# Kernel tuning notes

Hardware: AMD Instinct MI355X
Metric: run time of the kernel (lower is better)

The kernel has to match this reference:

```python
import jax, jax.numpy as jnp
import numpy as np

D_MODEL = 128
N_HEADS = 4
HEAD_DIM = D_MODEL // N_HEADS
N_LAYERS = 6
N_CELLS = 121
LN_EPS = 1e-5


def _build_hex_edges():
    # 11x11 axial hex grid -> 121 cells with 6-neighbor connectivity (640 directed edges)
    dirs = [(1, 0), (-1, 0), (0, 1), (0, -1), (1, -1), (-1, 1)]
    qr_to_idx = {(q, r): q * 11 + r for q in range(11) for r in range(11)}
    src, dst = [], []
    for (q, r), i in qr_to_idx.items():
        for dq, dr in dirs:
            j = qr_to_idx.get((q + dq, r + dr))
            if j is not None:
                src.append(i)
                dst.append(j)
    return jnp.array([src, dst], dtype=jnp.int32)


def layer_norm(x, g, b):
    m = jnp.mean(x, axis=-1, keepdims=True)
    v = jnp.mean(jnp.square(x - m), axis=-1, keepdims=True)
    return (x - m) * jax.lax.rsqrt(v + LN_EPS) * g + b


def gat_layer(h_in, edge_index, W, a_src, a_dst):
    # h_in: (B,N,d); W: (d, H*Dh); a_src/a_dst: (H,Dh)
    B, N, _ = h_in.shape
    h = (h_in @ W).reshape(B, N, N_HEADS, HEAD_DIM)
    src, dst = edge_index[0], edge_index[1]
    h_src = h[:, src]                                   # (B,E,H,Dh)
    e_src = jnp.einsum('behd,hd->beh', h_src, a_src)
    e_dst = jnp.einsum('behd,hd->beh', h[:, dst], a_dst)
    e = jax.nn.leaky_relu(e_src + e_dst, 0.2)           # (B,E,H)
    # edge softmax grouped by destination node (segment ops reduce leading axis)
    e_t = jnp.moveaxis(e, 1, 0)                         # (E,B,H)
    m = jax.ops.segment_max(e_t, dst, num_segments=N)   # (N,B,H)
    exp_e = jnp.exp(e_t - m[dst])                       # (E,B,H)
    s = jax.ops.segment_sum(exp_e, dst, num_segments=N) # (N,B,H)
    alpha = exp_e / (s[dst] + 1e-10)                    # (E,B,H)
    msgs = alpha[..., None] * jnp.moveaxis(h_src, 1, 0) # (E,B,H,Dh)
    out = jax.ops.segment_sum(msgs, dst, num_segments=N)  # (N,B,H,Dh)
    return jnp.moveaxis(out, 0, 1).reshape(B, N, N_HEADS * HEAD_DIM)


def _forward(x, enc_W, enc_b, enc_ln_g, enc_ln_b, ln1_g, ln1_b, gat_W, a_src, a_dst,
             ln2_g, ln2_b, ff_W1, ff_b1, ff_W2, ff_b2, fn_g, fn_b, edge_index):
    h = jax.nn.gelu(layer_norm(x @ enc_W + enc_b, enc_ln_g, enc_ln_b), approximate=False)
    for i in range(N_LAYERS):
        h = h + gat_layer(layer_norm(h, ln1_g[i], ln1_b[i]), edge_index,
                          gat_W[i], a_src[i], a_dst[i])
        hn = layer_norm(h, ln2_g[i], ln2_b[i])
        h = h + (jax.nn.gelu(hn @ ff_W1[i] + ff_b1[i], approximate=False) @ ff_W2[i] + ff_b2[i])
    return layer_norm(h, fn_g, fn_b)


def setup_inputs() -> dict:
    key = jax.random.key(0)
    ks = jax.random.split(key, 12)
    B, d, L, H, Dh = 256, D_MODEL, N_LAYERS, N_HEADS, HEAD_DIM
    inp = {
        'x': jax.random.uniform(ks[0], (B, N_CELLS, 6), dtype=jnp.float32),
        'enc_W': jax.random.normal(ks[1], (6, d), dtype=jnp.float32) * 0.3,
        'enc_b': jnp.zeros((d,), jnp.float32),
        'enc_ln_g': jnp.ones((d,), jnp.float32),
        'enc_ln_b': jnp.zeros((d,), jnp.float32),
        'ln1_g': jnp.ones((L, d), jnp.float32),
        'ln1_b': jnp.zeros((L, d), jnp.float32),
        'gat_W': jax.random.normal(ks[2], (L, d, H * Dh), dtype=jnp.float32) * (1.0 / np.sqrt(d)),
        'a_src': jax.random.normal(ks[3], (L, H, Dh), dtype=jnp.float32) * 0.1,
        'a_dst': jax.random.normal(ks[4], (L, H, Dh), dtype=jnp.float32) * 0.1,
        'ln2_g': jnp.ones((L, d), jnp.float32),
        'ln2_b': jnp.zeros((L, d), jnp.float32),
        'ff_W1': jax.random.normal(ks[5], (L, d, 4 * d), dtype=jnp.float32) * (1.0 / np.sqrt(d)),
        'ff_b1': jnp.zeros((L, 4 * d), jnp.float32),
        'ff_W2': jax.random.normal(ks[6], (L, 4 * d, d), dtype=jnp.float32) * (1.0 / np.sqrt(4 * d)),
        'ff_b2': jnp.zeros((L, d), jnp.float32),
        'fn_g': jnp.ones((d,), jnp.float32),
        'fn_b': jnp.zeros((d,), jnp.float32),
        'edge_index': _build_hex_edges(),
    }
    return inp


def reference(x, enc_W, enc_b, enc_ln_g, enc_ln_b, ln1_g, ln1_b, gat_W, a_src, a_dst,
              ln2_g, ln2_b, ff_W1, ff_b1, ff_W2, ff_b2, fn_g, fn_b, edge_index):
    return _forward(x, enc_W, enc_b, enc_ln_g, enc_ln_b, ln1_g, ln1_b, gat_W, a_src,
                    a_dst, ln2_g, ln2_b, ff_W1, ff_b1, ff_W2, ff_b2, fn_g, fn_b, edge_index)
```

## Files before the change

### kernel.cpp

```cpp
#include <hip/hip_runtime.h>
#include <math.h>

#define NCELL 121
#define NB 256
#define DMODEL 128
#define DFF 512
#define LNEPS 1e-5f
#define MAXDEG 8
#define ROWS (NB * NCELL)

typedef __attribute__((ext_vector_type(8))) short short8;
typedef __attribute__((ext_vector_type(4))) float f32x4;

#define MFMA(a, b, c) __builtin_amdgcn_mfma_f32_16x16x32_bf16(a, b, c, 0, 0, 0)

__device__ __forceinline__ float warp_sum64(float x) {
#pragma unroll
  for (int m = 32; m >= 1; m >>= 1) x += __shfl_xor(x, m, 64);
  return x;
}
__device__ __forceinline__ unsigned short f2bf(float f) {
  union { float f; unsigned u; } v; v.f = f;
  unsigned r = v.u + 0x7fffu + ((v.u >> 16) & 1u);
  return (unsigned short)(r >> 16);
}
__device__ __forceinline__ unsigned pack2(float a, float b) {
  return (unsigned)f2bf(a) | ((unsigned)f2bf(b) << 16);
}
__device__ __forceinline__ float bf2f(short s) {
  union { unsigned u; float f; } v;
  v.u = ((unsigned)(unsigned short)s) << 16;
  return v.f;
}
__device__ __forceinline__ float erf_fast(float x) {
  const float ax = fabsf(x);
  const float t = 1.0f / (1.0f + 0.3275911f * ax);
  const float p = t * (0.254829592f +
                  t * (-0.284496736f +
                  t * (1.421413741f +
                  t * (-1.453152027f +
                  t * 1.061405429f))));
  const float r = 1.0f - p * __expf(-ax * ax);
  return copysignf(r, x);
}
__device__ __forceinline__ float gelu_fast(float x) {
  return 0.5f * x * (1.0f + erf_fast(x * 0.70710678118654752f));
}
__device__ __forceinline__ float lrelu(float x) { return x > 0.0f ? x : 0.2f * x; }

__global__ void k_cvt(const float* __restrict__ src, short* __restrict__ dst,
                      int K, int N, int total) {
  const int i = blockIdx.x * 256 + threadIdx.x;
  if (i >= total) return;
  const int KN = K * N;
  const int layer = i / KN, rem = i % KN;
  const int n = rem / K, kk = rem % K;
  dst[i] = (short)f2bf(src[(size_t)layer * KN + (size_t)kk * N + n]);
}

__global__ void k_adj(const int* __restrict__ ei, int E,
                      int* __restrict__ deg, int* __restrict__ nbr) {
  const int node = blockIdx.x * 4 + (threadIdx.x >> 6);
  const int l = threadIdx.x & 63;
  if (node >= NCELL) return;
  const int* srcp = ei;
  const int* dstp = ei + E;
  int d = 0;
  for (int e0 = 0; e0 < E; e0 += 64) {
    const int e = e0 + l;
    const bool hit = (e < E) && (dstp[e] == node);
    const unsigned long long mb = __ballot(hit);
    if (hit) {
      const int pos = d + __popcll(mb & ((1ULL << l) - 1ULL));
      if (pos < MAXDEG) nbr[node * MAXDEG + pos] = srcp[e];
    }
    d += __popcll(mb);
  }
  if (l == 0) deg[node] = (d < MAXDEG ? d : MAXDEG);
}

__global__ __launch_bounds__(256) void k_enc(
    const float* __restrict__ x, const float* __restrict__ W,
    const float* __restrict__ bias, const float* __restrict__ g,
    const float* __restrict__ be, float* __restrict__ h) {
  const int tid = threadIdx.x, w = tid >> 6, l = tid & 63;
  const int r0 = blockIdx.x * 64;
  for (int k = 0; k < 16; k++) {
    const int gr = r0 + w * 16 + k;
    const float* xr = x + (size_t)gr * 6;
    const float x0 = xr[0], x1 = xr[1], x2 = xr[2];
    const float x3 = xr[3], x4 = xr[4], x5 = xr[5];
    const int d1 = l + 64;
    float v0 = bias[l] + x0 * W[l] + x1 * W[DMODEL + l] + x2 * W[2 * DMODEL + l]
             + x3 * W[3 * DMODEL + l] + x4 * W[4 * DMODEL + l] + x5 * W[5 * DMODEL + l];
    float v1 = bias[d1] + x0 * W[d1] + x1 * W[DMODEL + d1] + x2 * W[2 * DMODEL + d1]
             + x3 * W[3 * DMODEL + d1] + x4 * W[4 * DMODEL + d1] + x5 * W[5 * DMODEL + d1];
    const float mean = warp_sum64(v0 + v1) * (1.0f / 128.0f);
    const float e0 = v0 - mean, e1 = v1 - mean;
    const float var = warp_sum64(e0 * e0 + e1 * e1) * (1.0f / 128.0f);
    const float rs = rsqrtf(var + LNEPS);
    float* hp = h + (size_t)gr * DMODEL;
    hp[l] = gelu_fast(e0 * rs * g[l] + be[l]);
    hp[d1] = gelu_fast(e1 * rs * g[d1] + be[d1]);
  }
}

__global__ __launch_bounds__(256, 2) void k_gat_a(
    const float* __restrict__ g1, const float* __restrict__ b1,
    const short* __restrict__ Wgt, const float* __restrict__ asrc,
    const float* __restrict__ adst, const float* __restrict__ h,
    short* __restrict__ hh, float* __restrict__ es, float* __restrict__ ed) {
  __shared__ short sHn[64 * DMODEL];
  const int tid = threadIdx.x, w = tid >> 6, l = tid & 63;
  const int lane16 = l & 15, q = l >> 4;
  const int r0 = blockIdx.x * 64;

  {
    const int row = tid >> 2, sub = tid & 3;
    const float* hr = h + (size_t)(r0 + row) * DMODEL + sub * 32;
    float4 v[8];
#pragma unroll
    for (int i = 0; i < 8; i++) v[i] = ((const float4*)hr)[i];
    float s = 0.f, ss = 0.f;
#pragma unroll
    for (int i = 0; i < 8; i++) {
      s += (v[i].x + v[i].y) + (v[i].z + v[i].w);
      ss += v[i].x * v[i].x + v[i].y * v[i].y + v[i].z * v[i].z + v[i].w * v[i].w;
    }
    s += __shfl_xor(s, 1, 64);  s += __shfl_xor(s, 2, 64);
    ss += __shfl_xor(ss, 1, 64); ss += __shfl_xor(ss, 2, 64);
    const float mean = s * (1.0f / 128.0f);
    const float var = fmaxf(ss * (1.0f / 128.0f) - mean * mean, 0.0f);
    const float rs = rsqrtf(var + LNEPS);
    const float4* gp = (const float4*)(g1 + sub * 32);
    const float4* bp = (const float4*)(b1 + sub * 32);
    const int sw = (row & 7) << 3;
#pragma unroll
    for (int jj = 0; jj < 4; jj++) {
      const float4 ga = gp[jj * 2], gb = gp[jj * 2 + 1];
      const float4 ba = bp[jj * 2], bb = bp[jj * 2 + 1];
      const float4 va = v[jj * 2], vb = v[jj * 2 + 1];
      uint4 u;
      u.x = pack2((va.x - mean) * rs * ga.x + ba.x, (va.y - mean) * rs * ga.y + ba.y);
      u.y = pack2((va.z - mean) * rs * ga.z + ba.z, (va.w - mean) * rs * ga.w + ba.w);
      u.z = pack2((vb.x - mean) * rs * gb.x + bb.x, (vb.y - mean) * rs * gb.y + bb.y);
      u.w = pack2((vb.z - mean) * rs * gb.z + bb.z, (vb.w - mean) * rs * gb.w + bb.w);
      *(uint4*)&sHn[row * DMODEL + ((sub * 32 + jj * 8) ^ sw)] = u;
    }
  }
  __syncthreads();

  f32x4 acc[4][2];
#pragma unroll
  for (int m = 0; m < 4; m++)
#pragma unroll
    for (int n = 0; n < 2; n++) acc[m][n] = (f32x4){0.f, 0.f, 0.f, 0.f};
#pragma unroll
  for (int ks = 0; ks < 4; ks++) {
    short8 a[4];
#pragma unroll
    for (int m = 0; m < 4; m++) {
      const int row = m * 16 + lane16;
      a[m] = *(const short8*)&sHn[row * DMODEL + ((ks * 32 + q * 8) ^ ((row & 7) << 3))];
    }
#pragma unroll
    for (int n = 0; n < 2; n++) {
      const short8 b = *(const short8*)&Wgt[(size_t)(w * 32 + n * 16 + lane16) * DMODEL + ks * 32 + q * 8];
#pragma unroll
      for (int m = 0; m < 4; m++) acc[m][n] = MFMA(a[m], b, acc[m][n]);
    }
  }

  const float as0 = asrc[w * 32 + lane16], as1 = asrc[w * 32 + 16 + lane16];
  const float ad0 = adst[w * 32 + lane16], ad1 = adst[w * 32 + 16 + lane16];
#pragma unroll
  for (int m = 0; m < 4; m++) {
#pragma unroll
    for (int n = 0; n < 2; n++) {
      const int col = w * 32 + n * 16 + lane16;
#pragma unroll
      for (int r = 0; r < 4; r++) {
        const int row = m * 16 + q * 4 + r;
        hh[(size_t)(r0 + row) * DMODEL + col] = (short)f2bf(acc[m][n][r]);
      }
    }
#pragma unroll
    for (int r = 0; r < 4; r++) {
      float ps = acc[m][0][r] * as0 + acc[m][1][r] * as1;
      float pd = acc[m][0][r] * ad0 + acc[m][1][r] * ad1;
#pragma unroll
      for (int msk = 1; msk < 16; msk <<= 1) {
        ps += __shfl_xor(ps, msk, 64);
        pd += __shfl_xor(pd, msk, 64);
      }
      if (lane16 == 0) {
        const int gr = r0 + m * 16 + q * 4 + r;
        es[gr * 4 + w] = ps;
        ed[gr * 4 + w] = pd;
      }
    }
  }
}

__global__ __launch_bounds__(256) void k_gat_b(
    const float* __restrict__ es, const float* __restrict__ ed,
    const short* __restrict__ hh, const int* __restrict__ deg,
    const int* __restrict__ nbr, const float* __restrict__ g2,
    const float* __restrict__ bln, float* __restrict__ h,
    short* __restrict__ hn2) {
  const int tid = threadIdx.x, w = tid >> 6, l = tid & 63;
  const int task = blockIdx.x * 4 + w;
  const int b = task / NCELL;
  const int j = task - b * NCELL;
  const int base = b * NCELL;
  const int dg = deg[j];

  const int n_own = l >> 2, hd_own = l & 3;
  int gi_own = base;
  float e_val = -1e30f;
  if (n_own < dg) {
    gi_own = base + nbr[j * MAXDEG + n_own];
    e_val = lrelu(es[gi_own * 4 + hd_own] + ed[task * 4 + hd_own]);
  }
  float mx = e_val;
#pragma unroll
  for (int msk = 4; msk < 64; msk <<= 1) mx = fmaxf(mx, __shfl_xor(mx, msk, 64));
  float ex = (n_own < dg) ? __expf(e_val - mx) : 0.0f;
  float sm = ex;
#pragma unroll
  for (int msk = 4; msk < 64; msk <<= 1) sm += __shfl_xor(sm, msk, 64);
  const float wnorm = ex / (sm + 1e-10f);

  const int h0 = l >> 5, h2 = h0 + 2;
  float a0 = 0.0f, a1 = 0.0f;
  for (int n = 0; n < dg; n++) {
    const int gi = __shfl(gi_own, n * 4, 64);
    const float w0 = __shfl(wnorm, n * 4 + h0, 64);
    const float w2 = __shfl(wnorm, n * 4 + h2, 64);
    a0 = fmaf(w0, bf2f(hh[(size_t)gi * DMODEL + l]), a0);
    a1 = fmaf(w2, bf2f(hh[(size_t)gi * DMODEL + 64 + l]), a1);
  }
  float* hp = h + (size_t)task * DMODEL;
  const float v0 = hp[l] + a0;
  const float v1 = hp[l + 64] + a1;
  hp[l] = v0;
  hp[l + 64] = v1;

  const float mean = warp_sum64(v0 + v1) * (1.0f / 128.0f);
  const float e0 = v0 - mean, e1 = v1 - mean;
  const float var = warp_sum64(e0 * e0 + e1 * e1) * (1.0f / 128.0f);
  const float rs = rsqrtf(var + LNEPS);
  const int sw = (task & 7) << 3;
  hn2[(size_t)task * DMODEL + (l ^ sw)] = (short)f2bf(e0 * rs * g2[l] + bln[l]);
  hn2[(size_t)task * DMODEL + ((l + 64) ^ sw)] = (short)f2bf(e1 * rs * g2[l + 64] + bln[l + 64]);
}

__global__ __launch_bounds__(256, 4) void k_ffn(
    const short* __restrict__ hn2,
    const short* __restrict__ W1t, const float* __restrict__ bb1,
    const short* __restrict__ W2t, const float* __restrict__ bb2,
    float* __restrict__ h) {
  __shared__ short sHn[32 * DMODEL];
  __shared__ short sT[32 * DFF];
  const int tid = threadIdx.x, w = tid >> 6, l = tid & 63;
  const int lane16 = l & 15, q = l >> 4;
  const int r0 = blockIdx.x * 32;

  {
    const short* src = hn2 + (size_t)r0 * DMODEL;
#pragma unroll
    for (int i = 0; i < 2; i++) {
      const int off = (tid + i * 256) * 8;
      *(short8*)&sHn[off] = *(const short8*)&src[off];
    }
  }
  __syncthreads();

  f32x4 acc[2][8];
#pragma unroll
  for (int m = 0; m < 2; m++)
#pragma unroll
    for (int n = 0; n < 8; n++) acc[m][n] = (f32x4){0.f, 0.f, 0.f, 0.f};
#pragma unroll
  for (int ks = 0; ks < 4; ks++) {
    short8 a[2];
#pragma unroll
    for (int m = 0; m < 2; m++) {
      const int row = m * 16 + lane16;
      a[m] = *(const short8*)&sHn[row * DMODEL + ((ks * 32 + q * 8) ^ ((row & 7) << 3))];
    }
#pragma unroll
    for (int n = 0; n < 8; n++) {
      const short8 b = *(const short8*)&W1t[(size_t)(w * 128 + n * 16 + lane16) * DMODEL + ks * 32 + q * 8];
#pragma unroll
      for (int m = 0; m < 2; m++) acc[m][n] = MFMA(a[m], b, acc[m][n]);
    }
  }
#pragma unroll
  for (int m = 0; m < 2; m++)
#pragma unroll
    for (int n = 0; n < 8; n++) {
      const int col = w * 128 + n * 16 + lane16;
      const float bb = bb1[col];
#pragma unroll
      for (int r = 0; r < 4; r++) {
        const int row = m * 16 + q * 4 + r;
        sT[row * DFF + (col ^ ((row & 7) << 3))] = (short)f2bf(gelu_fast(acc[m][n][r] + bb));
      }
    }
  __syncthreads();

  f32x4 o[2][2];
#pragma unroll
  for (int m = 0; m < 2; m++)
#pragma unroll
    for (int n = 0; n < 2; n++) o[m][n] = (f32x4){0.f, 0.f, 0.f, 0.f};
#pragma unroll
  for (int ks = 0; ks < 16; ks++) {
    short8 a[2];
#pragma unroll
    for (int m = 0; m < 2; m++) {
      const int row = m * 16 + lane16;
      a[m] = *(const short8*)&sT[row * DFF + ((ks * 32 + q * 8) ^ ((row & 7) << 3))];
    }
#pragma unroll
    for (int n = 0; n < 2; n++) {
      const short8 b = *(const short8*)&W2t[(size_t)(w * 32 + n * 16 + lane16) * DFF + ks * 32 + q * 8];
#pragma unroll
      for (int m = 0; m < 2; m++) o[m][n] = MFMA(a[m], b, o[m][n]);
    }
  }
#pragma unroll
  for (int m = 0; m < 2; m++)
#pragma unroll
    for (int n = 0; n < 2; n++) {
      const int col = w * 32 + n * 16 + lane16;
      const float bb = bb2[col];
#pragma unroll
      for (int r = 0; r < 4; r++) {
        const int row = m * 16 + q * 4 + r;
        float* hp = h + (size_t)(r0 + row) * DMODEL + col;
        *hp = o[m][n][r] + bb + *hp;
      }
    }
}

__global__ __launch_bounds__(256) void k_final(
    const float* __restrict__ g, const float* __restrict__ be,
    float* __restrict__ h) {
  const int tid = threadIdx.x;
  const int row = tid >> 2, sub = tid & 3;
  const int gr = blockIdx.x * 64 + row;
  float* hr = h + (size_t)gr * DMODEL + sub * 32;
  float4 v[8];
#pragma unroll
  for (int i = 0; i < 8; i++) v[i] = ((const float4*)hr)[i];
  float s = 0.f, ss = 0.f;
#pragma unroll
  for (int i = 0; i < 8; i++) {
    s += (v[i].x + v[i].y) + (v[i].z + v[i].w);
    ss += v[i].x * v[i].x + v[i].y * v[i].y + v[i].z * v[i].z + v[i].w * v[i].w;
  }
  s += __shfl_xor(s, 1, 64);  s += __shfl_xor(s, 2, 64);
  ss += __shfl_xor(ss, 1, 64); ss += __shfl_xor(ss, 2, 64);
  const float mean = s * (1.0f / 128.0f);
  const float var = fmaxf(ss * (1.0f / 128.0f) - mean * mean, 0.0f);
  const float rs = rsqrtf(var + LNEPS);
  const float4* gp = (const float4*)(g + sub * 32);
  const float4* bp = (const float4*)(be + sub * 32);
#pragma unroll
  for (int i = 0; i < 8; i++) {
    const float4 gg = gp[i], bb = bp[i];
    float4 y;
    y.x = (v[i].x - mean) * rs * gg.x + bb.x;
    y.y = (v[i].y - mean) * rs * gg.y + bb.y;
    y.z = (v[i].z - mean) * rs * gg.z + bb.z;
    y.w = (v[i].w - mean) * rs * gg.w + bb.w;
    ((float4*)hr)[i] = y;
  }
}

extern "C" void kernel_launch(void* const* d_in, const int* in_sizes, int n_in,
                              void* d_out, int out_size, void* d_ws, size_t ws_size,
                              hipStream_t stream) {
  const float* x     = (const float*)d_in[0];
  const float* encW  = (const float*)d_in[1];
  const float* encb  = (const float*)d_in[2];
  const float* encg  = (const float*)d_in[3];
  const float* encbe = (const float*)d_in[4];
  const float* ln1g  = (const float*)d_in[5];
  const float* ln1b  = (const float*)d_in[6];
  const float* gatW  = (const float*)d_in[7];
  const float* a_src = (const float*)d_in[8];
  const float* a_dst = (const float*)d_in[9];
  const float* ln2g  = (const float*)d_in[10];
  const float* ln2b  = (const float*)d_in[11];
  const float* ffW1  = (const float*)d_in[12];
  const float* ffb1  = (const float*)d_in[13];
  const float* ffW2  = (const float*)d_in[14];
  const float* ffb2  = (const float*)d_in[15];
  const float* fng   = (const float*)d_in[16];
  const float* fnb   = (const float*)d_in[17];
  const int*   ei    = (const int*)d_in[18];
  const int E = in_sizes[18] / 2;

  float* h = (float*)d_out;
  char* ws = (char*)d_ws;
  int* nbr = (int*)ws;
  int* deg = nbr + NCELL * MAXDEG;
  short* wgt = (short*)(ws + 4608);
  short* w1t = wgt + 6 * DMODEL * DMODEL;
  short* w2t = w1t + 6 * DFF * DMODEL;
  short* hh  = w2t + 6 * DFF * DMODEL;
  short* hn2 = hh + (size_t)ROWS * DMODEL;
  float* es  = (float*)(hn2 + (size_t)ROWS * DMODEL);
  float* ed  = es + (size_t)ROWS * 4;

  k_cvt<<<dim3((6 * 16384 + 255) / 256), dim3(256), 0, stream>>>(gatW, wgt, 128, 128, 6 * 16384);
  k_cvt<<<dim3((6 * 65536 + 255) / 256), dim3(256), 0, stream>>>(ffW1, w1t, 128, 512, 6 * 65536);
  k_cvt<<<dim3((6 * 65536 + 255) / 256), dim3(256), 0, stream>>>(ffW2, w2t, 512, 128, 6 * 65536);
  k_adj<<<dim3((NCELL + 3) / 4), dim3(256), 0, stream>>>(ei, E, deg, nbr);

  k_enc<<<dim3(ROWS / 64), dim3(256), 0, stream>>>(x, encW, encb, encg, encbe, h);
  for (int lyr = 0; lyr < 6; lyr++) {
    k_gat_a<<<dim3(ROWS / 64), dim3(256), 0, stream>>>(
        ln1g + lyr * DMODEL, ln1b + lyr * DMODEL,
        wgt + lyr * DMODEL * DMODEL,
        a_src + lyr * DMODEL, a_dst + lyr * DMODEL,
        h, hh, es, ed);
    k_gat_b<<<dim3(ROWS / 4), dim3(256), 0, stream>>>(
        es, ed, hh, deg, nbr,
        ln2g + lyr * DMODEL, ln2b + lyr * DMODEL, h, hn2);
    k_ffn<<<dim3(ROWS / 32), dim3(256), 0, stream>>>(
        hn2,
        w1t + lyr * DFF * DMODEL, ffb1 + lyr * DFF,
        w2t + lyr * DFF * DMODEL, ffb2 + lyr * DMODEL,
        h);
  }
  k_final<<<dim3(ROWS / 64), dim3(256), 0, stream>>>(fng, fnb, h);
}
```

Measured before the change: 486.8 us.

## Fuse GAT aggregation, LayerNorm and FFN into one kernel per layer

Merges the attention-softmax aggregation kernel into the FFN kernel. Each 32-row block now computes the residual and LayerNorm2 directly into shared memory instead of round-tripping hn2 and h through global memory. This removes one launch per layer and the global write and read of the normalized activations. In exchange there is more shared memory per block (an extra fp32 tile), lower occupancy (launch bounds set to 2 blocks), and the gather phase has less parallelism per block.

```diff
diff --git a/kernel.cpp b/kernel.cpp
--- a/kernel.cpp
+++ b/kernel.cpp
@@ -8,6 +8,7 @@
 #define LNEPS 1e-5f
 #define MAXDEG 8
 #define ROWS (NB * NCELL)
+#define SH32_LD 132
 
 typedef __attribute__((ext_vector_type(8))) short short8;
 typedef __attribute__((ext_vector_type(4))) float f32x4;
@@ -202,147 +203,139 @@
   }
 }
 
-__global__ __launch_bounds__(256) void k_gat_b(
+__global__ __launch_bounds__(256, 2) void k_fuse(
     const float* __restrict__ es, const float* __restrict__ ed,
     const short* __restrict__ hh, const int* __restrict__ deg,
-    const int* __restrict__ nbr, const float* __restrict__ g2,
-    const float* __restrict__ bln, float* __restrict__ h,
-    short* __restrict__ hn2) {
-  const int tid = threadIdx.x, w = tid >> 6, l = tid & 63;
-  const int task = blockIdx.x * 4 + w;
-  const int b = task / NCELL;
-  const int j = task - b * NCELL;
-  const int base = b * NCELL;
-  const int dg = deg[j];
-
-  const int n_own = l >> 2, hd_own = l & 3;
-  int gi_own = base;
-  float e_val = -1e30f;
-  if (n_own < dg) {
-    gi_own = base + nbr[j * MAXDEG + n_own];
-    e_val = lrelu(es[gi_own * 4 + hd_own] + ed[task * 4 + hd_own]);
-  }
-  float mx = e_val;
-#pragma unroll
-  for (int msk = 4; msk < 64; msk <<= 1) mx = fmaxf(mx, __shfl_xor(mx, msk, 64));
-  float ex = (n_own < dg) ? __expf(e_val - mx) : 0.0f;
-  float sm = ex;
-#pragma unroll
-  for (int msk = 4; msk < 64; msk <<= 1) sm += __shfl_xor(sm, msk, 64);
-  const float wnorm = ex / (sm + 1e-10f);
-
-  const int h0 = l >> 5, h2 = h0 + 2;
-  float a0 = 0.0f, a1 = 0.0f;
-  for (int n = 0; n < dg; n++) {
-    const int gi = __shfl(gi_own, n * 4, 64);
-    const float w0 = __shfl(wnorm, n * 4 + h0, 64);
-    const float w2 = __shfl(wnorm, n * 4 + h2, 64);
-    a0 = fmaf(w0, bf2f(hh[(size_t)gi * DMODEL + l]), a0);
-    a1 = fmaf(w2, bf2f(hh[(size_t)gi * DMODEL + 64 + l]), a1);
-  }
-  float* hp = h + (size_t)task * DMODEL;
-  const float v0 = hp[l] + a0;
-  const float v1 = hp[l + 64] + a1;
-  hp[l] = v0;
-  hp[l + 64] = v1;
-
-  const float mean = warp_sum64(v0 + v1) * (1.0f / 128.0f);
-  const float e0 = v0 - mean, e1 = v1 - mean;
-  const float var = warp_sum64(e0 * e0 + e1 * e1) * (1.0f / 128.0f);
-  const float rs = rsqrtf(var + LNEPS);
-  const int sw = (task & 7) << 3;
-  hn2[(size_t)task * DMODEL + (l ^ sw)] = (short)f2bf(e0 * rs * g2[l] + bln[l]);
-  hn2[(size_t)task * DMODEL + ((l + 64) ^ sw)] = (short)f2bf(e1 * rs * g2[l + 64] + bln[l + 64]);
-}
-
-__global__ __launch_bounds__(256, 4) void k_ffn(
-    const short* __restrict__ hn2,
+    const int* __restrict__ nbr,
+    const float* __restrict__ g2, const float* __restrict__ bln,
     const short* __restrict__ W1t, const float* __restrict__ bb1,
     const short* __restrict__ W2t, const float* __restrict__ bb2,
     float* __restrict__ h) {
   __shared__ short sHn[32 * DMODEL];
   __shared__ short sT[32 * DFF];
+  __shared__ float sH32[32 * SH32_LD];
   const int tid = threadIdx.x, w = tid >> 6, l = tid & 63;
   const int lane16 = l & 15, q = l >> 4;
   const int r0 = blockIdx.x * 32;
 
+  const int n_own = l >> 2, hd_own = l & 3;
+  const int h0 = l >> 5, h2 = h0 + 2;
+  for (int t = 0; t < 8; t++) {
+    const int trow = w * 8 + t;
+    const int gr = r0 + trow;
+    const int b = gr / NCELL;
+    const int j = gr - b * NCELL;
+    const int base = b * NCELL;
+    const int dg = deg[j];
+    int gi_own = base;
+    float e_val = -1e30f;
+    if (n_own < dg) {
+      gi_own = base + nbr[j * MAXDEG + n_own];
+      e_val = lrelu(es[gi_own * 4 + hd_own] + ed[gr * 4 + hd_own]);
+    }
+    float mx = e_val;
+#pragma unroll
+    for (int msk = 4; msk < 64; msk <<= 1) mx = fmaxf(mx, __shfl_xor(mx, msk, 64));
+    float ex = (n_own < dg) ? __expf(e_val - mx) : 0.0f;
+    float sm = ex;
+#pragma unroll
+    for (int msk = 4; msk < 64; msk <<= 1) sm += __shfl_xor(sm, msk, 64);
+    const float wnorm = ex / (sm + 1e-10f);
+
+    float a0 = 0.0f, a1 = 0.0f;
+    for (int n = 0; n < dg; n++) {
+      const int gi = __shfl(gi_own, n * 4, 64);
+      const float w0 = __shfl(wnorm, n * 4 + h0, 64);
+      const float w2 = __shfl(wnorm, n * 4 + h2, 64);
+      a0 = fmaf(w0, bf2f(hh[(size_t)gi * DMODEL + l]), a0);
+      a1 = fmaf(w2, bf2f(hh[(size_t)gi * DMODEL + 64 + l]), a1);
+    }
+    const float* hp = h + (size_t)gr * DMODEL;
+    const float v0 = hp[l] + a0;
+    const float v1 = hp[l + 64] + a1;
+    sH32[trow * SH32_LD + l] = v0;
+    sH32[trow * SH32_LD + l + 64] = v1;
+
+    const float mean = warp_sum64(v0 + v1) * (1.0f / 128.0f);
+    const float e0 = v0 - mean, e1 = v1 - mean;
+    const float var = warp_sum64(e0 * e0 + e1 * e1) * (1.0f / 128.0f);
+    const float rs = rsqrtf(var + LNEPS);
+    const int sw = (trow & 7) << 3;
+    sHn[trow * DMODEL + (l ^ sw)] = (short)f2bf((v0 - mean) * rs * g2[l] + bln[l]);
+    sHn[trow * DMODEL + ((l + 64) ^ sw)] = (short)f2bf((v1 - mean) * rs * g2[l + 64] + bln[l + 64]);
+  }
+  __syncthreads();
+
   {
-    const short* src = hn2 + (size_t)r0 * DMODEL;
-#pragma unroll
-    for (int i = 0; i < 2; i++) {
-      const int off = (tid + i * 256) * 8;
-      *(short8*)&sHn[off] = *(const short8*)&src[off];
-    }
+    f32x4 acc[2][8];
+#pragma unroll
+    for (int m = 0; m < 2; m++)
+#pragma unroll
+      for (int n = 0; n < 8; n++) acc[m][n] = (f32x4){0.f, 0.f, 0.f, 0.f};
+#pragma unroll
+    for (int ks = 0; ks < 4; ks++) {
+      short8 a[2];
+#pragma unroll
+      for (int m = 0; m < 2; m++) {
+        const int row = m * 16 + lane16;
+        a[m] = *(const short8*)&sHn[row * DMODEL + ((ks * 32 + q * 8) ^ ((row & 7) << 3))];
+      }
+#pragma unroll
+      for (int n = 0; n < 8; n++) {
+        const short8 b = *(const short8*)&W1t[(size_t)(w * 128 + n * 16 + lane16) * DMODEL + ks * 32 + q * 8];
+#pragma unroll
+        for (int m = 0; m < 2; m++) acc[m][n] = MFMA(a[m], b, acc[m][n]);
+      }
+    }
+#pragma unroll
+    for (int m = 0; m < 2; m++)
+#pragma unroll
+      for (int n = 0; n < 8; n++) {
+        const int col = w * 128 + n * 16 + lane16;
+        const float bb = bb1[col];
+#pragma unroll
+        for (int r = 0; r < 4; r++) {
+          const int row = m * 16 + q * 4 + r;
+          sT[row * DFF + (col ^ ((row & 7) << 3))] = (short)f2bf(gelu_fast(acc[m][n][r] + bb));
+        }
+      }
   }
   __syncthreads();
 
-  f32x4 acc[2][8];
-#pragma unroll
-  for (int m = 0; m < 2; m++)
-#pragma unroll
-    for (int n = 0; n < 8; n++) acc[m][n] = (f32x4){0.f, 0.f, 0.f, 0.f};
-#pragma unroll
-  for (int ks = 0; ks < 4; ks++) {
-    short8 a[2];
-#pragma unroll
-    for (int m = 0; m < 2; m++) {
-      const int row = m * 16 + lane16;
-      a[m] = *(const short8*)&sHn[row * DMODEL + ((ks * 32 + q * 8) ^ ((row & 7) << 3))];
-    }
-#pragma unroll
-    for (int n = 0; n < 8; n++) {
-      const short8 b = *(const short8*)&W1t[(size_t)(w * 128 + n * 16 + lane16) * DMODEL + ks * 32 + q * 8];
-#pragma unroll
-      for (int m = 0; m < 2; m++) acc[m][n] = MFMA(a[m], b, acc[m][n]);
-    }
-  }
-#pragma unroll
-  for (int m = 0; m < 2; m++)
-#pragma unroll
-    for (int n = 0; n < 8; n++) {
-      const int col = w * 128 + n * 16 + lane16;
-      const float bb = bb1[col];
-#pragma unroll
-      for (int r = 0; r < 4; r++) {
-        const int row = m * 16 + q * 4 + r;
-        sT[row * DFF + (col ^ ((row & 7) << 3))] = (short)f2bf(gelu_fast(acc[m][n][r] + bb));
-      }
-    }
-  __syncthreads();
-
-  f32x4 o[2][2];
-#pragma unroll
-  for (int m = 0; m < 2; m++)
-#pragma unroll
-    for (int n = 0; n < 2; n++) o[m][n] = (f32x4){0.f, 0.f, 0.f, 0.f};
-#pragma unroll
-  for (int ks = 0; ks < 16; ks++) {
-    short8 a[2];
-#pragma unroll
-    for (int m = 0; m < 2; m++) {
-      const int row = m * 16 + lane16;
-      a[m] = *(const short8*)&sT[row * DFF + ((ks * 32 + q * 8) ^ ((row & 7) << 3))];
-    }
-#pragma unroll
-    for (int n = 0; n < 2; n++) {
-      const short8 b = *(const short8*)&W2t[(size_t)(w * 32 + n * 16 + lane16) * DFF + ks * 32 + q * 8];
-#pragma unroll
-      for (int m = 0; m < 2; m++) o[m][n] = MFMA(a[m], b, o[m][n]);
-    }
-  }
-#pragma unroll
-  for (int m = 0; m < 2; m++)
-#pragma unroll
-    for (int n = 0; n < 2; n++) {
-      const int col = w * 32 + n * 16 + lane16;
-      const float bb = bb2[col];
-#pragma unroll
-      for (int r = 0; r < 4; r++) {
-        const int row = m * 16 + q * 4 + r;
-        float* hp = h + (size_t)(r0 + row) * DMODEL + col;
-        *hp = o[m][n][r] + bb + *hp;
-      }
-    }
+  {
+    f32x4 o[2][2];
+#pragma unroll
+    for (int m = 0; m < 2; m++)
+#pragma unroll
+      for (int n = 0; n < 2; n++) o[m][n] = (f32x4){0.f, 0.f, 0.f, 0.f};
+#pragma unroll
+    for (int ks = 0; ks < 16; ks++) {
+      short8 a[2];
+#pragma unroll
+      for (int m = 0; m < 2; m++) {
+        const int row = m * 16 + lane16;
+        a[m] = *(const short8*)&sT[row * DFF + ((ks * 32 + q * 8) ^ ((row & 7) << 3))];
+      }
+#pragma unroll
+      for (int n = 0; n < 2; n++) {
+        const short8 b = *(const short8*)&W2t[(size_t)(w * 32 + n * 16 + lane16) * DFF + ks * 32 + q * 8];
+#pragma unroll
+        for (int m = 0; m < 2; m++) o[m][n] = MFMA(a[m], b, o[m][n]);
+      }
+    }
+#pragma unroll
+    for (int m = 0; m < 2; m++)
+#pragma unroll
+      for (int n = 0; n < 2; n++) {
+        const int col = w * 32 + n * 16 + lane16;
+        const float bb = bb2[col];
+#pragma unroll
+        for (int r = 0; r < 4; r++) {
+          const int row = m * 16 + q * 4 + r;
+          h[(size_t)(r0 + row) * DMODEL + col] = o[m][n][r] + bb + sH32[row * SH32_LD + col];
+        }
+      }
+  }
 }
 
 __global__ __launch_bounds__(256) void k_final(
@@ -412,8 +405,7 @@
   short* w1t = wgt + 6 * DMODEL * DMODEL;
   short* w2t = w1t + 6 * DFF * DMODEL;
   short* hh  = w2t + 6 * DFF * DMODEL;
-  short* hn2 = hh + (size_t)ROWS * DMODEL;
-  float* es  = (float*)(hn2 + (size_t)ROWS * DMODEL);
+  float* es  = (float*)(hh + (size_t)ROWS * DMODEL);
   float* ed  = es + (size_t)ROWS * 4;
 
   k_cvt<<<dim3((6 * 16384 + 255) / 256), dim3(256), 0, stream>>>(gatW, wgt, 128, 128, 6 * 16384);
@@ -422,20 +414,22 @@
   k_adj<<<dim3((NCELL + 3) / 4), dim3(256), 0, stream>>>(ei, E, deg, nbr);
 
   k_enc<<<dim3(ROWS / 64), dim3(256), 0, stream>>>(x, encW, encb, encg, encbe, h);
-  for (int lyr = 0; lyr < 6; lyr++) {
-    k_gat_a<<<dim3(ROWS / 64), dim3(256), 0, stream>>>(
-        ln1g + lyr * DMODEL, ln1b + lyr * DMODEL,
-        wgt + lyr * DMODEL * DMODEL,
-        a_src + lyr * DMODEL, a_dst + lyr * DMODEL,
-        h, hh, es, ed);
-    k_gat_b<<<dim3(ROWS / 4), dim3(256), 0, stream>>>(
+  k_gat_a<<<dim3(ROWS / 64), dim3(256), 0, stream>>>(
+      ln1g, ln1b, wgt, a_src, a_dst, h, hh, es, ed);
+  for (int i = 0; i < 6; i++) {
+    k_fuse<<<dim3(ROWS / 32), dim3(256), 0, stream>>>(
         es, ed, hh, deg, nbr,
-        ln2g + lyr * DMODEL, ln2b + lyr * DMODEL, h, hn2);
-    k_ffn<<<dim3(ROWS / 32), dim3(256), 0, stream>>>(
-        hn2,
-        w1t + lyr * DFF * DMODEL, ffb1 + lyr * DFF,
-        w2t + lyr * DFF * DMODEL, ffb2 + lyr * DMODEL,
+        ln2g + i * DMODEL, ln2b + i * DMODEL,
+        w1t + i * DFF * DMODEL, ffb1 + i * DFF,
+        w2t + i * DFF * DMODEL, ffb2 + i * DMODEL,
         h);
+    if (i < 5) {
+      k_gat_a<<<dim3(ROWS / 64), dim3(256), 0, stream>>>(
+          ln1g + (i + 1) * DMODEL, ln1b + (i + 1) * DMODEL,
+          wgt + (i + 1) * DMODEL * DMODEL,
+          a_src + (i + 1) * DMODEL, a_dst + (i + 1) * DMODEL,
+          h, hh, es, ed);
+    }
   }
   k_final<<<dim3(ROWS / 64), dim3(256), 0, stream>>>(fng, fnb, h);
 }
```

Result: slower. 649.8 us (+33.5%).
